# Kernel tuning notes

Measured on AMD Instinct MI355X. Metric: run time of the kernel, lower is better.

Reference implementation:

```python
import jax, jax.numpy as jnp
import numpy as np

N_NODES = 50000
N_EDGES = 800000
IN_DIM = 256
OUT_DIM = 64
NEG_SLOPE = 0.01  # torch F.leaky_relu default


def setup_inputs() -> dict:
    key = jax.random.key(0)
    k1, k2, k3, k4, k5 = jax.random.split(key, 5)
    return {
        "h": jax.random.normal(k1, (N_NODES, IN_DIM), dtype=jnp.float32),
        "src": jax.random.randint(k2, (N_EDGES,), 0, N_NODES, dtype=jnp.int32),
        "dst": jax.random.randint(k3, (N_EDGES,), 0, N_NODES, dtype=jnp.int32),
        "W_fc": jax.random.normal(k4, (IN_DIM, OUT_DIM), dtype=jnp.float32) / np.sqrt(IN_DIM),
        "a_vec": jax.random.normal(k5, (2 * OUT_DIM,), dtype=jnp.float32) / np.sqrt(2 * OUT_DIM),
    }


def reference(h, src, dst, W_fc, a_vec):
    n = h.shape[0]
    d = W_fc.shape[1]
    # z = fc(h)
    z = h @ W_fc  # [N, out_dim]
    # edge attention: attn_fc(cat[z_src, z_dst]) == z_src@a[:d] + z_dst@a[d:]
    s_src = z @ a_vec[:d]  # [N]
    s_dst = z @ a_vec[d:]  # [N]
    e = jax.nn.leaky_relu(s_src[src] + s_dst[dst], negative_slope=NEG_SLOPE)  # [E]
    # segment softmax over incoming edges of each dst node (stable)
    e_max = jax.ops.segment_max(e, dst, num_segments=n)  # -inf for isolated nodes (unused)
    e_exp = jnp.exp(e - e_max[dst])
    denom = jax.ops.segment_sum(e_exp, dst, num_segments=n)
    alpha = e_exp / denom[dst]  # [E]
    # weighted scatter-sum of source features
    out = jax.ops.segment_sum(alpha[:, None] * z[src], dst, num_segments=n)  # [N, out_dim]
    return out
```

## Files before the change

### kernel.cpp

```cpp
#include <hip/hip_runtime.h>

#define IN_DIM 256
#define OUT_DIM 64
#define NEG_SLOPE 0.01f
#define SCAN_CHUNK 2048
#define HBS 280

typedef short short8 __attribute__((ext_vector_type(8)));
typedef float f32x4 __attribute__((ext_vector_type(4)));
typedef unsigned short u16x4 __attribute__((ext_vector_type(4)));
typedef unsigned short u16x8 __attribute__((ext_vector_type(8)));

__device__ __forceinline__ unsigned short f2b(float f) {
    unsigned u = __float_as_uint(f);
    return (unsigned short)((u + 0x7FFFu + ((u >> 16) & 1u)) >> 16);
}
__device__ __forceinline__ float b2f(unsigned short b) {
    return __uint_as_float(((unsigned)b) << 16);
}

__global__ __launch_bounds__(256) void gemm_mfma(const float* __restrict__ h,
                                                 const float* __restrict__ W,
                                                 const float* __restrict__ a,
                                                 unsigned short* __restrict__ zb,
                                                 float* __restrict__ s_src,
                                                 float* __restrict__ s_dst,
                                                 int* __restrict__ deg, int ndeg, int n) {
    __shared__ unsigned short hb[64 * HBS];
    __shared__ unsigned short wb[64 * HBS];
    __shared__ float sp1[2][64];
    __shared__ float sp2[2][64];
    const int tid = threadIdx.x;
    const int lane = tid & 63;
    const int w = tid >> 6;
    const int row0 = blockIdx.x * 64;

    if (tid < 66) {
        int di = blockIdx.x * 66 + tid;
        if (di < ndeg) deg[di] = 0;
    }

    {
        int c4 = (tid & 15) * 4;
        int kb = (tid >> 4) * 16;
        #pragma unroll
        for (int kk = 0; kk < 16; ++kk) {
            int k = kb + kk;
            float4 wv = *(const float4*)&W[(size_t)k * OUT_DIM + c4];
            wb[(c4 + 0) * HBS + k] = f2b(wv.x);
            wb[(c4 + 1) * HBS + k] = f2b(wv.y);
            wb[(c4 + 2) * HBS + k] = f2b(wv.z);
            wb[(c4 + 3) * HBS + k] = f2b(wv.w);
        }
    }
    {
        int r = tid >> 2, seg = tid & 3;
        int grow = row0 + r;
        #pragma unroll
        for (int i = 0; i < 16; ++i) {
            float4 hv = make_float4(0.f, 0.f, 0.f, 0.f);
            if (grow < n)
                hv = *(const float4*)&h[(size_t)grow * IN_DIM + seg * 64 + i * 4];
            u16x4 p;
            p[0] = f2b(hv.x); p[1] = f2b(hv.y); p[2] = f2b(hv.z); p[3] = f2b(hv.w);
            *(u16x4*)&hb[r * HBS + seg * 64 + i * 4] = p;
        }
    }
    __syncthreads();

    const int rw = (w & 1) * 32;
    const int cw = (w >> 1) * 32;
    const int l16 = lane & 15;
    const int q = lane >> 4;

    f32x4 acc[2][2] = {};
    #pragma unroll
    for (int ks = 0; ks < 8; ++ks) {
        short8 af[2], bf[2];
        #pragma unroll
        for (int i = 0; i < 2; ++i)
            af[i] = *(const short8*)&hb[(rw + i * 16 + l16) * HBS + ks * 32 + q * 8];
        #pragma unroll
        for (int j = 0; j < 2; ++j)
            bf[j] = *(const short8*)&wb[(cw + j * 16 + l16) * HBS + ks * 32 + q * 8];
        #pragma unroll
        for (int i = 0; i < 2; ++i)
            #pragma unroll
            for (int j = 0; j < 2; ++j)
                acc[i][j] = __builtin_amdgcn_mfma_f32_16x16x32_bf16(af[i], bf[j], acc[i][j], 0, 0, 0);
    }

    #pragma unroll
    for (int i = 0; i < 2; ++i) {
        #pragma unroll
        for (int reg = 0; reg < 4; ++reg) {
            int row_local = rw + i * 16 + q * 4 + reg;
            int grow = row0 + row_local;
            float p1 = 0.f, p2 = 0.f;
            #pragma unroll
            for (int j = 0; j < 2; ++j) {
                int col = cw + j * 16 + l16;
                float zv = acc[i][j][reg];
                if (grow < n) zb[(size_t)grow * OUT_DIM + col] = f2b(zv);
                p1 = fmaf(zv, a[col], p1);
                p2 = fmaf(zv, a[OUT_DIM + col], p2);
            }
            #pragma unroll
            for (int o = 1; o < 16; o <<= 1) {
                p1 += __shfl_xor(p1, o);
                p2 += __shfl_xor(p2, o);
            }
            if (l16 == 0) {
                sp1[w >> 1][row_local] = p1;
                sp2[w >> 1][row_local] = p2;
            }
        }
    }
    __syncthreads();
    if (tid < 64) {
        int grow = row0 + tid;
        if (grow < n) {
            s_src[grow] = sp1[0][tid] + sp1[1][tid];
            s_dst[grow] = sp2[0][tid] + sp2[1][tid];
        }
    }
}

__global__ __launch_bounds__(256) void count_deg(const int* __restrict__ dst,
                                                 int* __restrict__ deg,
                                                 int* __restrict__ rank, int E) {
    int i = blockIdx.x * 256 + threadIdx.x;
    if (i >= E) return;
    rank[i] = atomicAdd(&deg[dst[i]], 1);
}

__global__ __launch_bounds__(256) void scan_sums(const int* __restrict__ deg,
                                                 int* __restrict__ bsum,
                                                 int* __restrict__ ebase,
                                                 int* __restrict__ offs,
                                                 int* __restrict__ ticket, int n, int nb) {
    __shared__ int red[256];
    __shared__ int lastFlag;
    const int tid = threadIdx.x;
    int base = blockIdx.x * SCAN_CHUNK + tid * 8;
    int s = 0;
    #pragma unroll
    for (int j = 0; j < 8; ++j)
        if (base + j < n) s += deg[base + j];
    red[tid] = s;
    __syncthreads();
    #pragma unroll
    for (int d = 128; d; d >>= 1) {
        if (tid < d) red[tid] += red[tid + d];
        __syncthreads();
    }
    if (tid == 0) {
        bsum[blockIdx.x] = red[0];
        __threadfence();
        int t = atomicAdd(ticket, 1);
        lastFlag = (t == nb - 1);
    }
    __syncthreads();
    if (lastFlag && tid == 0) {
        int run = 0;
        for (int b = 0; b < nb; ++b) {
            int v = atomicAdd(&bsum[b], 0);
            ebase[b] = run;
            run += v;
        }
        offs[n] = run;
    }
}

__global__ __launch_bounds__(256) void scan_local(const int* __restrict__ deg,
                                                  const int* __restrict__ ebase,
                                                  int* __restrict__ offs, int n) {
    __shared__ int ts[256];
    const int tid = threadIdx.x;
    int base = blockIdx.x * SCAN_CHUNK + tid * 8;
    int v[8];
    int s = 0;
    #pragma unroll
    for (int j = 0; j < 8; ++j) {
        v[j] = (base + j < n) ? deg[base + j] : 0;
        s += v[j];
    }
    ts[tid] = s;
    __syncthreads();
    #pragma unroll
    for (int d = 1; d < 256; d <<= 1) {
        int add = (tid >= d) ? ts[tid - d] : 0;
        __syncthreads();
        ts[tid] += add;
        __syncthreads();
    }
    int run = ebase[blockIdx.x] + ts[tid] - s;
    #pragma unroll
    for (int j = 0; j < 8; ++j) {
        if (base + j < n) offs[base + j] = run;
        run += v[j];
    }
}

__global__ __launch_bounds__(256) void scatter_csr(const int* __restrict__ src,
                                                   const int* __restrict__ dst,
                                                   const float* __restrict__ s_src,
                                                   const float* __restrict__ s_dst,
                                                   const int* __restrict__ offs,
                                                   const int* __restrict__ rank,
                                                   int2* __restrict__ csr, int E) {
    int i = blockIdx.x * 256 + threadIdx.x;
    if (i >= E) return;
    int s = src[i], t = dst[i];
    float x = s_src[s] + s_dst[t];
    x = x > 0.f ? x : NEG_SLOPE * x;
    float w = __expf(x);
    int pos = offs[t] + rank[i];
    csr[pos] = make_int2(s, __float_as_int(w));
}

__global__ __launch_bounds__(256) void aggregate(const int* __restrict__ offs,
                                                 const int2* __restrict__ csr,
                                                 const unsigned short* __restrict__ zb,
                                                 float* __restrict__ out, int n) {
    int node = blockIdx.x * 4 + (threadIdx.x >> 6);
    int lane = threadIdx.x & 63;
    if (node >= n) return;
    const int q = lane >> 3;
    const int l = lane & 7;
    int beg = offs[node];
    int end = offs[node + 1];

    float acc[8] = {};
    float s = 0.f;
    int j = beg + q;
    for (; j + 8 < end; j += 16) {
        int2 e0 = csr[j];
        int2 e1 = csr[j + 8];
        float w0 = __int_as_float(e0.y);
        float w1 = __int_as_float(e1.y);
        u16x8 z0 = *(const u16x8*)&zb[(size_t)e0.x * OUT_DIM + l * 8];
        u16x8 z1 = *(const u16x8*)&zb[(size_t)e1.x * OUT_DIM + l * 8];
        #pragma unroll
        for (int k = 0; k < 8; ++k) {
            acc[k] = fmaf(w0, b2f(z0[k]), acc[k]);
            acc[k] = fmaf(w1, b2f(z1[k]), acc[k]);
        }
        s += w0 + w1;
    }
    for (; j < end; j += 8) {
        int2 e0 = csr[j];
        float w0 = __int_as_float(e0.y);
        u16x8 z0 = *(const u16x8*)&zb[(size_t)e0.x * OUT_DIM + l * 8];
        #pragma unroll
        for (int k = 0; k < 8; ++k) acc[k] = fmaf(w0, b2f(z0[k]), acc[k]);
        s += w0;
    }
    #pragma unroll
    for (int o = 8; o < 64; o <<= 1) {
        #pragma unroll
        for (int k = 0; k < 8; ++k) acc[k] += __shfl_xor(acc[k], o);
        s += __shfl_xor(s, o);
    }
    if (q == 0) {
        float inv = (end > beg) ? 1.0f / s : 0.f;
        float4 o0 = make_float4(acc[0] * inv, acc[1] * inv, acc[2] * inv, acc[3] * inv);
        float4 o1 = make_float4(acc[4] * inv, acc[5] * inv, acc[6] * inv, acc[7] * inv);
        *(float4*)&out[(size_t)node * OUT_DIM + l * 8] = o0;
        *(float4*)&out[(size_t)node * OUT_DIM + l * 8 + 4] = o1;
    }
}

extern "C" void kernel_launch(void* const* d_in, const int* in_sizes, int n_in,
                              void* d_out, int out_size, void* d_ws, size_t ws_size,
                              hipStream_t stream) {
    const float* h   = (const float*)d_in[0];
    const int*   src = (const int*)d_in[1];
    const int*   dst = (const int*)d_in[2];
    const float* W   = (const float*)d_in[3];
    const float* a   = (const float*)d_in[4];
    float* out = (float*)d_out;

    const int n = in_sizes[0] / IN_DIM;
    const int E = in_sizes[1];
    const int nb = (n + SCAN_CHUNK - 1) / SCAN_CHUNK;

    char* ws = (char*)d_ws;
    size_t off_b = 0;
    auto alloc = [&](size_t bytes) -> void* {
        void* p = ws + off_b;
        off_b += (bytes + 255) & ~(size_t)255;
        return p;
    };
    unsigned short* zb    = (unsigned short*)alloc((size_t)n * OUT_DIM * sizeof(unsigned short));
    float*          s_src = (float*)alloc((size_t)n * sizeof(float));
    float*          s_dst = (float*)alloc((size_t)n * sizeof(float));
    int*            deg   = (int*)alloc((size_t)(n + 64) * sizeof(int));
    int*            ticket= deg + n;
    int*            offs  = (int*)alloc((size_t)(n + 1) * sizeof(int));
    int*            rank  = (int*)alloc((size_t)E * sizeof(int));
    int*            bsum  = (int*)alloc(256 * sizeof(int));
    int*            ebase = (int*)alloc(256 * sizeof(int));
    int2*           csr   = (int2*)alloc((size_t)E * sizeof(int2));

    const int ndeg = n + 64;

    gemm_mfma<<<(n + 63) / 64, 256, 0, stream>>>(h, W, a, zb, s_src, s_dst, deg, ndeg, n);
    count_deg<<<(E + 255) / 256, 256, 0, stream>>>(dst, deg, rank, E);
    scan_sums<<<nb, 256, 0, stream>>>(deg, bsum, ebase, offs, ticket, n, nb);
    scan_local<<<nb, 256, 0, stream>>>(deg, ebase, offs, n);
    scatter_csr<<<(E + 255) / 256, 256, 0, stream>>>(src, dst, s_src, s_dst, offs,
                                                     rank, csr, E);
    aggregate<<<(n + 3) / 4, 256, 0, stream>>>(offs, csr, zb, out, n);
}
```

Before: 195.3 us.

## Fuse scan kernels with grid flag and vectorize edge kernels and GEMM staging

The two-pass prefix scan is merged into one kernel. The last block to arrive computes the block bases and sets a global flag, and the other blocks spin on that flag before writing their offsets. This removes one kernel launch and one round trip through global memory. The degree-count and CSR-scatter kernels now handle four edges per thread using int4 loads. The GEMM staging of W and h is rewritten to write 8-wide bf16 vectors into shared memory, at the cost of scalar strided W loads. The spin-wait relies on every scan block being resident at once, and the quartered launch grid assumes E is a multiple of four.

```diff
diff --git a/kernel.cpp b/kernel.cpp
--- a/kernel.cpp
+++ b/kernel.cpp
@@ -8,7 +8,6 @@
 
 typedef short short8 __attribute__((ext_vector_type(8)));
 typedef float f32x4 __attribute__((ext_vector_type(4)));
-typedef unsigned short u16x4 __attribute__((ext_vector_type(4)));
 typedef unsigned short u16x8 __attribute__((ext_vector_type(8)));
 
 __device__ __forceinline__ unsigned short f2b(float f) {
@@ -41,29 +40,33 @@
     }
 
     {
-        int c4 = (tid & 15) * 4;
-        int kb = (tid >> 4) * 16;
-        #pragma unroll
-        for (int kk = 0; kk < 16; ++kk) {
-            int k = kb + kk;
-            float4 wv = *(const float4*)&W[(size_t)k * OUT_DIM + c4];
-            wb[(c4 + 0) * HBS + k] = f2b(wv.x);
-            wb[(c4 + 1) * HBS + k] = f2b(wv.y);
-            wb[(c4 + 2) * HBS + k] = f2b(wv.z);
-            wb[(c4 + 3) * HBS + k] = f2b(wv.w);
+        int c = tid & 63, kseg = tid >> 6;
+        #pragma unroll
+        for (int i = 0; i < 8; ++i) {
+            u16x8 p;
+            #pragma unroll
+            for (int j = 0; j < 8; ++j) {
+                int k = kseg * 64 + i * 8 + j;
+                p[j] = f2b(W[(size_t)k * OUT_DIM + c]);
+            }
+            *(u16x8*)&wb[c * HBS + kseg * 64 + i * 8] = p;
         }
     }
     {
-        int r = tid >> 2, seg = tid & 3;
+        int r = tid & 63, seg = tid >> 6;
         int grow = row0 + r;
         #pragma unroll
-        for (int i = 0; i < 16; ++i) {
-            float4 hv = make_float4(0.f, 0.f, 0.f, 0.f);
-            if (grow < n)
-                hv = *(const float4*)&h[(size_t)grow * IN_DIM + seg * 64 + i * 4];
-            u16x4 p;
-            p[0] = f2b(hv.x); p[1] = f2b(hv.y); p[2] = f2b(hv.z); p[3] = f2b(hv.w);
-            *(u16x4*)&hb[r * HBS + seg * 64 + i * 4] = p;
+        for (int i = 0; i < 8; ++i) {
+            float4 h0 = make_float4(0.f, 0.f, 0.f, 0.f);
+            float4 h1 = make_float4(0.f, 0.f, 0.f, 0.f);
+            if (grow < n) {
+                h0 = *(const float4*)&h[(size_t)grow * IN_DIM + seg * 64 + i * 8];
+                h1 = *(const float4*)&h[(size_t)grow * IN_DIM + seg * 64 + i * 8 + 4];
+            }
+            u16x8 p;
+            p[0] = f2b(h0.x); p[1] = f2b(h0.y); p[2] = f2b(h0.z); p[3] = f2b(h0.w);
+            p[4] = f2b(h1.x); p[5] = f2b(h1.y); p[6] = f2b(h1.z); p[7] = f2b(h1.w);
+            *(u16x8*)&hb[r * HBS + seg * 64 + i * 8] = p;
         }
     }
     __syncthreads();
@@ -129,53 +132,29 @@
 __global__ __launch_bounds__(256) void count_deg(const int* __restrict__ dst,
                                                  int* __restrict__ deg,
                                                  int* __restrict__ rank, int E) {
-    int i = blockIdx.x * 256 + threadIdx.x;
-    if (i >= E) return;
-    rank[i] = atomicAdd(&deg[dst[i]], 1);
-}
-
-__global__ __launch_bounds__(256) void scan_sums(const int* __restrict__ deg,
-                                                 int* __restrict__ bsum,
-                                                 int* __restrict__ ebase,
-                                                 int* __restrict__ offs,
-                                                 int* __restrict__ ticket, int n, int nb) {
-    __shared__ int red[256];
-    __shared__ int lastFlag;
-    const int tid = threadIdx.x;
-    int base = blockIdx.x * SCAN_CHUNK + tid * 8;
-    int s = 0;
-    #pragma unroll
-    for (int j = 0; j < 8; ++j)
-        if (base + j < n) s += deg[base + j];
-    red[tid] = s;
-    __syncthreads();
-    #pragma unroll
-    for (int d = 128; d; d >>= 1) {
-        if (tid < d) red[tid] += red[tid + d];
-        __syncthreads();
-    }
-    if (tid == 0) {
-        bsum[blockIdx.x] = red[0];
-        __threadfence();
-        int t = atomicAdd(ticket, 1);
-        lastFlag = (t == nb - 1);
-    }
-    __syncthreads();
-    if (lastFlag && tid == 0) {
-        int run = 0;
-        for (int b = 0; b < nb; ++b) {
-            int v = atomicAdd(&bsum[b], 0);
-            ebase[b] = run;
-            run += v;
-        }
-        offs[n] = run;
-    }
-}
-
-__global__ __launch_bounds__(256) void scan_local(const int* __restrict__ deg,
-                                                  const int* __restrict__ ebase,
-                                                  int* __restrict__ offs, int n) {
+    int base = (blockIdx.x * 256 + threadIdx.x) * 4;
+    if (base >= E) return;
+    if (base + 3 < E) {
+        int4 tv = *(const int4*)&dst[base];
+        int4 rv;
+        rv.x = atomicAdd(&deg[tv.x], 1);
+        rv.y = atomicAdd(&deg[tv.y], 1);
+        rv.z = atomicAdd(&deg[tv.z], 1);
+        rv.w = atomicAdd(&deg[tv.w], 1);
+        *(int4*)&rank[base] = rv;
+    } else {
+        for (int i = base; i < E; ++i) rank[i] = atomicAdd(&deg[dst[i]], 1);
+    }
+}
+
+__global__ __launch_bounds__(256) void scan_fused(const int* __restrict__ deg,
+                                                  int* __restrict__ bsum,
+                                                  int* __restrict__ ebase,
+                                                  int* __restrict__ offs,
+                                                  int* __restrict__ ticket,
+                                                  int* __restrict__ flag, int n, int nb) {
     __shared__ int ts[256];
+    __shared__ int base_sh;
     const int tid = threadIdx.x;
     int base = blockIdx.x * SCAN_CHUNK + tid * 8;
     int v[8];
@@ -194,7 +173,26 @@
         ts[tid] += add;
         __syncthreads();
     }
-    int run = ebase[blockIdx.x] + ts[tid] - s;
+    if (tid == 0) {
+        bsum[blockIdx.x] = ts[255];
+        __threadfence();
+        int t = atomicAdd(ticket, 1);
+        if (t == nb - 1) {
+            int run = 0;
+            for (int b = 0; b < nb; ++b) {
+                int vv = atomicAdd(&bsum[b], 0);
+                ebase[b] = run;
+                run += vv;
+            }
+            offs[n] = run;
+            __threadfence();
+            atomicExch(flag, 1);
+        }
+        while (atomicAdd(flag, 0) == 0) __builtin_amdgcn_s_sleep(8);
+        base_sh = atomicAdd(&ebase[blockIdx.x], 0);
+    }
+    __syncthreads();
+    int run = base_sh + ts[tid] - s;
     #pragma unroll
     for (int j = 0; j < 8; ++j) {
         if (base + j < n) offs[base + j] = run;
@@ -209,14 +207,29 @@
                                                    const int* __restrict__ offs,
                                                    const int* __restrict__ rank,
                                                    int2* __restrict__ csr, int E) {
-    int i = blockIdx.x * 256 + threadIdx.x;
-    if (i >= E) return;
-    int s = src[i], t = dst[i];
-    float x = s_src[s] + s_dst[t];
-    x = x > 0.f ? x : NEG_SLOPE * x;
-    float w = __expf(x);
-    int pos = offs[t] + rank[i];
-    csr[pos] = make_int2(s, __float_as_int(w));
+    int base = (blockIdx.x * 256 + threadIdx.x) * 4;
+    if (base >= E) return;
+    if (base + 3 < E) {
+        int4 sv = *(const int4*)&src[base];
+        int4 tv = *(const int4*)&dst[base];
+        int4 rv = *(const int4*)&rank[base];
+        #pragma unroll
+        for (int k = 0; k < 4; ++k) {
+            int s = (&sv.x)[k], t = (&tv.x)[k];
+            float x = s_src[s] + s_dst[t];
+            x = x > 0.f ? x : NEG_SLOPE * x;
+            float wgt = __expf(x);
+            csr[offs[t] + (&rv.x)[k]] = make_int2(s, __float_as_int(wgt));
+        }
+    } else {
+        for (int i = base; i < E; ++i) {
+            int s = src[i], t = dst[i];
+            float x = s_src[s] + s_dst[t];
+            x = x > 0.f ? x : NEG_SLOPE * x;
+            float wgt = __expf(x);
+            csr[offs[t] + rank[i]] = make_int2(s, __float_as_int(wgt));
+        }
+    }
 }
 
 __global__ __launch_bounds__(256) void aggregate(const int* __restrict__ offs,
@@ -297,6 +310,7 @@
     float*          s_dst = (float*)alloc((size_t)n * sizeof(float));
     int*            deg   = (int*)alloc((size_t)(n + 64) * sizeof(int));
     int*            ticket= deg + n;
+    int*            flag  = deg + n + 1;
     int*            offs  = (int*)alloc((size_t)(n + 1) * sizeof(int));
     int*            rank  = (int*)alloc((size_t)E * sizeof(int));
     int*            bsum  = (int*)alloc(256 * sizeof(int));
@@ -306,10 +320,9 @@
     const int ndeg = n + 64;
 
     gemm_mfma<<<(n + 63) / 64, 256, 0, stream>>>(h, W, a, zb, s_src, s_dst, deg, ndeg, n);
-    count_deg<<<(E + 255) / 256, 256, 0, stream>>>(dst, deg, rank, E);
-    scan_sums<<<nb, 256, 0, stream>>>(deg, bsum, ebase, offs, ticket, n, nb);
-    scan_local<<<nb, 256, 0, stream>>>(deg, ebase, offs, n);
-    scatter_csr<<<(E + 255) / 256, 256, 0, stream>>>(src, dst, s_src, s_dst, offs,
-                                                     rank, csr, E);
+    count_deg<<<(E / 4 + 255) / 256, 256, 0, stream>>>(dst, deg, rank, E);
+    scan_fused<<<nb, 256, 0, stream>>>(deg, bsum, ebase, offs, ticket, flag, n, nb);
+    scatter_csr<<<(E / 4 + 255) / 256, 256, 0, stream>>>(src, dst, s_src, s_dst, offs,
+                                                         rank, csr, E);
     aggregate<<<(n + 3) / 4, 256, 0, stream>>>(offs, csr, zb, out, n);
 }
```

New measurement: 196.0 us. Within noise of the previous version (+0.3%).
